# Kernel optimization log

Hardware: AMD Instinct MI355X
Metric: run time of the kernel (lower is better)

The kernel has to match this reference:

```python
import jax, jax.numpy as jnp
import numpy as np

D = 1024
H = 4096  # int(dim * mlp_ratio)
E = 8
B, N = 2, 2048


def setup_inputs() -> dict:
    key = jax.random.key(0)
    ks = jax.random.split(key, 5)
    x = jax.random.normal(ks[0], (B, N, D), dtype=jnp.float32)
    # torch Linear weights, stored pre-transposed for right-multiplication
    W1 = jax.random.normal(ks[1], (E, D, H), dtype=jnp.float32) / np.sqrt(D)
    W2 = jax.random.normal(ks[2], (E, H, D), dtype=jnp.float32) / np.sqrt(H)
    Wg = jax.random.normal(ks[3], (D, E), dtype=jnp.float32) / np.sqrt(D)
    bg = jax.random.normal(ks[4], (E,), dtype=jnp.float32) * 0.01
    return {"x": x, "W1": W1, "W2": W2, "Wg": Wg, "bg": bg}


def reference(x, W1, W2, Wg, bg):
    b, n, d = x.shape
    e = Wg.shape[1]
    xf = x.reshape(b * n, d)                      # [T, D]
    logits = xf @ Wg + bg                         # [T, E]
    one_hot = jax.nn.one_hot(jnp.argmax(logits, axis=-1), e, dtype=x.dtype)  # [T, E]
    # Dense all-experts compute (faithful to the original module)
    h = jax.nn.gelu(jnp.einsum('td,edh->eth', xf, W1), approximate=True)     # [E, T, H]
    y = jnp.einsum('eth,ehd->etd', h, W2)                                    # [E, T, D]
    out = jnp.einsum('etd,te->td', y, one_hot)                               # top-1 combine
    return out.reshape(b, n, d)
```

## Files before the change

kernel.cpp:

```cpp
#include <hip/hip_runtime.h>
#include <hip/hip_bf16.h>

#define Dq 1024
#define Hq 4096
#define Tq 4096
#define MAXTILES 40
#define NSTEP 16

#define XB_OFF 65536
#define HC_OFF (XB_OFF + Tq * Dq * 2)
#define WT_OFF (HC_OFF + MAXTILES * 128 * Hq * 2)

#define M_NT 0
#define M_CNT 8
#define M_POFF 16
#define M_CUR 32
#define M_TE 64
#define M_TR 128
#define M_EXP 512
#define M_PERM 4608

typedef __attribute__((ext_vector_type(8))) short bf16x8;
typedef __attribute__((ext_vector_type(4))) float f32x4;

__device__ __forceinline__ short f2bf(float f) {
    __hip_bfloat16 h = __float2bfloat16(f);
    return *reinterpret_cast<short*>(&h);
}

__device__ __forceinline__ float gelu_tanh(float x) {
    float u = 0.7978845608028654f * (x + 0.044715f * x * x * x);
    return x / (1.0f + __expf(-2.0f * u));
}

typedef __attribute__((address_space(1))) const void gvoid;
typedef __attribute__((address_space(3))) void lvoid;
__device__ __forceinline__ void glds16(const void* g, void* l) {
    __builtin_amdgcn_global_load_lds((gvoid*)g, (lvoid*)l, 16, 0, 0);
}

__global__ void k_init(int* meta) {
    int i = blockIdx.x * 256 + threadIdx.x;
    if (i < M_PERM + MAXTILES * 128) meta[i] = 0;
}

__global__ void k_tr(const float* __restrict__ in, short* __restrict__ out, int R, int C) {
    __shared__ float t[64][65];
    int e = blockIdx.z;
    int c0 = blockIdx.x * 64;
    int r0 = blockIdx.y * 64;
    const float* ine = in + (size_t)e * R * C;
    short* oute = out + (size_t)e * R * C;
    int tt = threadIdx.x;
    int lr = tt >> 4;
    int lc = (tt & 15) * 4;
#pragma unroll
    for (int p = 0; p < 4; ++p) {
        int r = p * 16 + lr;
        float4 v = *(const float4*)(ine + (size_t)(r0 + r) * C + c0 + lc);
        t[r][lc] = v.x; t[r][lc + 1] = v.y; t[r][lc + 2] = v.z; t[r][lc + 3] = v.w;
    }
    __syncthreads();
#pragma unroll
    for (int p = 0; p < 4; ++p) {
        int c = p * 16 + lr;
        short4 s;
        s.x = f2bf(t[lc][c]); s.y = f2bf(t[lc + 1][c]);
        s.z = f2bf(t[lc + 2][c]); s.w = f2bf(t[lc + 3][c]);
        *(short4*)(oute + (size_t)(c0 + c) * R + r0 + lc) = s;
    }
}

__global__ void k_route(const float* __restrict__ x, const float* __restrict__ Wg,
                        const float* __restrict__ bg, int* meta, short* __restrict__ xb) {
    int wave = threadIdx.x >> 6;
    int lane = threadIdx.x & 63;
    int t = blockIdx.x * 4 + wave;
    const float* xr = x + (size_t)t * Dq;
    float acc[8];
#pragma unroll
    for (int e = 0; e < 8; ++e) acc[e] = 0.0f;
#pragma unroll
    for (int j = 0; j < 16; ++j) {
        int d = j * 64 + lane;
        float xv = xr[d];
        xb[(size_t)t * Dq + d] = f2bf(xv);
        float4 w0 = *(const float4*)(Wg + (size_t)d * 8);
        float4 w1 = *(const float4*)(Wg + (size_t)d * 8 + 4);
        acc[0] += xv * w0.x; acc[1] += xv * w0.y; acc[2] += xv * w0.z; acc[3] += xv * w0.w;
        acc[4] += xv * w1.x; acc[5] += xv * w1.y; acc[6] += xv * w1.z; acc[7] += xv * w1.w;
    }
#pragma unroll
    for (int e = 0; e < 8; ++e) {
#pragma unroll
        for (int off = 32; off > 0; off >>= 1) acc[e] += __shfl_xor(acc[e], off);
    }
    if (lane == 0) {
        float best = acc[0] + bg[0];
        int be = 0;
#pragma unroll
        for (int e = 1; e < 8; ++e) {
            float v = acc[e] + bg[e];
            if (v > best) { best = v; be = e; }
        }
        meta[M_EXP + t] = be;
        atomicAdd(&meta[M_CNT + be], 1);
    }
}

__global__ void k_scan(int* meta) {
    if (threadIdx.x != 0) return;
    int off = 0, nt = 0;
    for (int e = 0; e < 8; ++e) {
        meta[M_POFF + e] = off;
        int c = meta[M_CNT + e];
        int m = (c + 127) / 128;
        for (int j = 0; j < m; ++j) {
            meta[M_TE + nt] = e;
            meta[M_TR + nt] = off + j * 128;
            ++nt;
        }
        off += m * 128;
    }
    meta[M_POFF + 8] = off;
    meta[M_NT] = nt;
}

__global__ void k_scatter(int* meta) {
    int t = blockIdx.x * 256 + threadIdx.x;
    if (t >= Tq) return;
    int e = meta[M_EXP + t];
    int pos = atomicAdd(&meta[M_CUR + e], 1);
    meta[M_PERM + meta[M_POFF + e] + pos] = t;
}

#define GEMM_SETUP()                                                           \
    int tt = threadIdx.x, w = tt >> 6, lane = tt & 63;                         \
    int fr = lane & 15, fg = lane >> 4;                                        \
    int rlo = lane >> 3;                                                       \
    int csw = ((lane & 7) ^ rlo) * 8;                                          \
    int ldsOff[4];                                                             \
    _Pragma("unroll")                                                          \
    for (int s = 0; s < 4; ++s) ldsOff[s] = (s * 32 + w * 8) * 64;             \
    int wm = (w >> 1) * 64, wn = (w & 1) * 64;                                 \
    int aoff[2][4], boff[2][4];                                                \
    _Pragma("unroll")                                                          \
    for (int s2 = 0; s2 < 2; ++s2)                                             \
      _Pragma("unroll")                                                        \
      for (int f = 0; f < 4; ++f) {                                            \
        int c = s2 * 4 + fg;                                                   \
        int m = wm + f * 16 + fr;                                              \
        aoff[s2][f] = m * 64 + ((c ^ (m & 7)) * 8);                            \
        int n = wn + f * 16 + fr;                                              \
        boff[s2][f] = n * 64 + ((c ^ (n & 7)) * 8);                            \
      }                                                                        \
    f32x4 acc[4][4];                                                           \
    _Pragma("unroll")                                                          \
    for (int a = 0; a < 4; ++a)                                                \
      _Pragma("unroll")                                                        \
      for (int b = 0; b < 4; ++b) acc[a][b] = (f32x4){0.f, 0.f, 0.f, 0.f};

#define KLOOP()                                                                \
  _Pragma("unroll")                                                            \
  for (int t = 0; t < NSTEP; ++t) {                                            \
    __syncthreads();                                                           \
    bf16x8 af[2][4], bv[2][4];                                                 \
    _Pragma("unroll")                                                          \
    for (int s2 = 0; s2 < 2; ++s2)                                             \
      _Pragma("unroll")                                                        \
      for (int f = 0; f < 4; ++f) {                                            \
        af[s2][f] = *(const bf16x8*)(&As[aoff[s2][f]]);                        \
        bv[s2][f] = *(const bf16x8*)(&Bs[boff[s2][f]]);                        \
      }                                                                        \
    __syncthreads();                                                           \
    if (t + 1 < NSTEP) {                                                       \
      _Pragma("unroll")                                                        \
      for (int s = 0; s < 4; ++s) {                                            \
        glds16(aSrc[s] + (t + 1) * 64, As + ldsOff[s]);                        \
        glds16(bSrc[s] + (t + 1) * 64, Bs + ldsOff[s]);                        \
      }                                                                        \
    }                                                                          \
    __builtin_amdgcn_sched_barrier(0);                                         \
    __builtin_amdgcn_s_setprio(1);                                             \
    _Pragma("unroll")                                                          \
    for (int s2 = 0; s2 < 2; ++s2)                                             \
      _Pragma("unroll")                                                        \
      for (int fm = 0; fm < 4; ++fm)                                           \
        _Pragma("unroll")                                                      \
        for (int fn = 0; fn < 4; ++fn)                                         \
          acc[fm][fn] = __builtin_amdgcn_mfma_f32_16x16x32_bf16(               \
              af[s2][fm], bv[s2][fn], acc[fm][fn], 0, 0, 0);                   \
    __builtin_amdgcn_s_setprio(0);                                             \
  }

__global__ __launch_bounds__(256, 3) void k_gemm1(const short* __restrict__ xb,
                                                  const short* __restrict__ W1T,
                                                  const int* __restrict__ meta,
                                                  short* __restrict__ Hc) {
    __shared__ short As[128 * 64];
    __shared__ short Bs[128 * 64];
    int hw = blockIdx.x;
    int xcd = hw & 7, q = hw >> 3;
    int mt = q >> 2;
    int n0 = (xcd * 4 + (q & 3)) * 128;
    if (mt >= meta[M_NT]) return;
    int e = meta[M_TE + mt];
    int i0 = meta[M_TR + mt];
    const int* perm = meta + M_PERM;

    GEMM_SETUP()

    const short* aSrc[4];
    const short* bSrc[4];
#pragma unroll
    for (int s = 0; s < 4; ++s) {
        int row = s * 32 + w * 8 + rlo;
        aSrc[s] = xb + (size_t)perm[i0 + row] * Dq + csw;
        bSrc[s] = W1T + ((size_t)e * Hq + n0 + row) * Dq + csw;
    }

#pragma unroll
    for (int s = 0; s < 4; ++s) {
        glds16(aSrc[s], As + ldsOff[s]);
        glds16(bSrc[s], Bs + ldsOff[s]);
    }

    KLOOP()

#pragma unroll
    for (int fm = 0; fm < 4; ++fm) {
        int rbase = i0 + wm + fm * 16 + fg * 4;
#pragma unroll
        for (int fn = 0; fn < 4; ++fn) {
            int col = n0 + wn + fn * 16 + fr;
#pragma unroll
            for (int p = 0; p < 4; ++p) {
                float v = gelu_tanh(acc[fm][fn][p]);
                Hc[(size_t)(rbase + p) * Hq + col] = f2bf(v);
            }
        }
    }
}

__global__ __launch_bounds__(256, 3) void k_gemm2(const short* __restrict__ Hc,
                                                  const short* __restrict__ W2T,
                                                  const int* __restrict__ meta,
                                                  float* __restrict__ out) {
    __shared__ short As[128 * 64];
    __shared__ short Bs[128 * 64];
    int hw = blockIdx.x;
    int xcd = hw & 7, q = hw >> 3;
    int mt = q >> 2;
    int sk = q & 3;
    int n0 = xcd * 128;
    int kbase = sk * (Hq / 4);
    if (mt >= meta[M_NT]) return;
    int e = meta[M_TE + mt];
    int i0 = meta[M_TR + mt];
    const int* perm = meta + M_PERM;
    int vend = meta[M_POFF + e] + meta[M_CNT + e];

    GEMM_SETUP()

    const short* aSrc[4];
    const short* bSrc[4];
#pragma unroll
    for (int s = 0; s < 4; ++s) {
        int row = s * 32 + w * 8 + rlo;
        aSrc[s] = Hc + (size_t)(i0 + row) * Hq + kbase + csw;
        bSrc[s] = W2T + ((size_t)e * Dq + n0 + row) * Hq + kbase + csw;
    }

#pragma unroll
    for (int s = 0; s < 4; ++s) {
        glds16(aSrc[s], As + ldsOff[s]);
        glds16(bSrc[s], Bs + ldsOff[s]);
    }

    KLOOP()

#pragma unroll
    for (int fm = 0; fm < 4; ++fm) {
        int rbase = i0 + wm + fm * 16 + fg * 4;
#pragma unroll
        for (int p = 0; p < 4; ++p) {
            int i = rbase + p;
            if (i < vend) {
                int tok = perm[i];
#pragma unroll
                for (int fn = 0; fn < 4; ++fn) {
                    int col = n0 + wn + fn * 16 + fr;
                    atomicAdd(&out[(size_t)tok * Dq + col], acc[fm][fn][p]);
                }
            }
        }
    }
}

extern "C" void kernel_launch(void* const* d_in, const int* in_sizes, int n_in,
                              void* d_out, int out_size, void* d_ws, size_t ws_size,
                              hipStream_t stream) {
    const float* x  = (const float*)d_in[0];
    const float* W1 = (const float*)d_in[1];
    const float* W2 = (const float*)d_in[2];
    const float* Wg = (const float*)d_in[3];
    const float* bg = (const float*)d_in[4];
    float* out = (float*)d_out;
    int* meta = (int*)d_ws;
    short* xb = (short*)((char*)d_ws + XB_OFF);
    short* Hc = (short*)((char*)d_ws + HC_OFF);
    short* WT = (short*)((char*)d_ws + WT_OFF);

    k_init<<<38, 256, 0, stream>>>(meta);
    hipMemsetAsync(d_out, 0, (size_t)Tq * Dq * 4, stream);
    k_route<<<Tq / 4, 256, 0, stream>>>(x, Wg, bg, meta, xb);
    k_scan<<<1, 64, 0, stream>>>(meta);
    k_scatter<<<Tq / 256, 256, 0, stream>>>(meta);
    k_tr<<<dim3(Hq / 64, Dq / 64, 8), 256, 0, stream>>>(W1, WT, Dq, Hq);
    k_gemm1<<<1280, 256, 0, stream>>>(xb, WT, meta, Hc);
    k_tr<<<dim3(Dq / 64, Hq / 64, 8), 256, 0, stream>>>(W2, WT, Hq, Dq);
    k_gemm2<<<1280, 256, 0, stream>>>(Hc, WT, meta, out);
}
```

Baseline: 294.4 us.

## Double-buffer LDS in grouped GEMMs and halve split-K in second GEMM

Both grouped GEMM kernels now use two LDS buffers, so the global-to-LDS loads for the next K step are issued before computing on the current one. The old scheme read fragments into registers and then synchronised before loading. Explicit vmcnt waits and raw barriers replace the paired __syncthreads. The K step is also split into two phases to cut register pressure. gemm1 remaps blocks so tiles sharing the same weight column group sit together, and gemm2 moves from 4-way to 2-way split-K with 640 blocks, reducing atomic traffic into the output. Occupancy drops from 3 to 2 blocks per CU because of the doubled LDS use.

Measured after the change: 310.0 us. 1.05x slower.

```diff
diff --git a/kernel.cpp b/kernel.cpp
--- a/kernel.cpp
+++ b/kernel.cpp
@@ -5,7 +5,6 @@
 #define Hq 4096
 #define Tq 4096
 #define MAXTILES 40
-#define NSTEP 16
 
 #define XB_OFF 65536
 #define HC_OFF (XB_OFF + Tq * Dq * 2)
@@ -38,6 +37,9 @@
 __device__ __forceinline__ void glds16(const void* g, void* l) {
     __builtin_amdgcn_global_load_lds((gvoid*)g, (lvoid*)l, 16, 0, 0);
 }
+
+#define WAITVM_(N) asm volatile("s_waitcnt vmcnt(" #N ")" ::: "memory")
+#define WAITVM(N) WAITVM_(N)
 
 __global__ void k_init(int* meta) {
     int i = blockIdx.x * 256 + threadIdx.x;
@@ -158,51 +160,60 @@
     _Pragma("unroll")                                                          \
     for (int a = 0; a < 4; ++a)                                                \
       _Pragma("unroll")                                                        \
-      for (int b = 0; b < 4; ++b) acc[a][b] = (f32x4){0.f, 0.f, 0.f, 0.f};
-
-#define KLOOP()                                                                \
-  _Pragma("unroll")                                                            \
-  for (int t = 0; t < NSTEP; ++t) {                                            \
-    __syncthreads();                                                           \
-    bf16x8 af[2][4], bv[2][4];                                                 \
-    _Pragma("unroll")                                                          \
-    for (int s2 = 0; s2 < 2; ++s2)                                             \
+      for (int b = 0; b < 2 * 2; ++b) acc[a][b] = (f32x4){0.f, 0.f, 0.f, 0.f};
+
+#define PHASE(S2, P)                                                           \
+  {                                                                            \
+    bf16x8 af[4], bv[4];                                                       \
+    _Pragma("unroll")                                                          \
+    for (int f = 0; f < 4; ++f) {                                              \
+      af[f] = *(const bf16x8*)(&As[(P) * 8192 + aoff[S2][f]]);                 \
+      bv[f] = *(const bf16x8*)(&Bs[(P) * 8192 + boff[S2][f]]);                 \
+    }                                                                          \
+    __builtin_amdgcn_s_barrier();                                              \
+    asm volatile("s_waitcnt lgkmcnt(0)" ::: "memory");                         \
+    __builtin_amdgcn_sched_barrier(0);                                         \
+    __builtin_amdgcn_s_setprio(1);                                             \
+    _Pragma("unroll")                                                          \
+    for (int fm = 0; fm < 4; ++fm)                                             \
       _Pragma("unroll")                                                        \
-      for (int f = 0; f < 4; ++f) {                                            \
-        af[s2][f] = *(const bf16x8*)(&As[aoff[s2][f]]);                        \
-        bv[s2][f] = *(const bf16x8*)(&Bs[boff[s2][f]]);                        \
-      }                                                                        \
-    __syncthreads();                                                           \
-    if (t + 1 < NSTEP) {                                                       \
+      for (int fn = 0; fn < 4; ++fn)                                           \
+        acc[fm][fn] = __builtin_amdgcn_mfma_f32_16x16x32_bf16(                 \
+            af[fm], bv[fn], acc[fm][fn], 0, 0, 0);                             \
+    __builtin_amdgcn_s_setprio(0);                                             \
+    __builtin_amdgcn_s_barrier();                                              \
+    asm volatile("" ::: "memory");                                             \
+  }
+
+#define KSTEP(T, NSTEP)                                                        \
+  {                                                                            \
+    const int P = (T) & 1;                                                     \
+    if ((T) + 1 < (NSTEP)) {                                                   \
       _Pragma("unroll")                                                        \
       for (int s = 0; s < 4; ++s) {                                            \
-        glds16(aSrc[s] + (t + 1) * 64, As + ldsOff[s]);                        \
-        glds16(bSrc[s] + (t + 1) * 64, Bs + ldsOff[s]);                        \
+        glds16(aSrc[s] + ((T) + 1) * 64, As + (1 - P) * 8192 + ldsOff[s]);     \
+        glds16(bSrc[s] + ((T) + 1) * 64, Bs + (1 - P) * 8192 + ldsOff[s]);     \
       }                                                                        \
+      WAITVM(8);                                                               \
+    } else {                                                                   \
+      WAITVM(0);                                                               \
     }                                                                          \
-    __builtin_amdgcn_sched_barrier(0);                                         \
-    __builtin_amdgcn_s_setprio(1);                                             \
-    _Pragma("unroll")                                                          \
-    for (int s2 = 0; s2 < 2; ++s2)                                             \
-      _Pragma("unroll")                                                        \
-      for (int fm = 0; fm < 4; ++fm)                                           \
-        _Pragma("unroll")                                                      \
-        for (int fn = 0; fn < 4; ++fn)                                         \
-          acc[fm][fn] = __builtin_amdgcn_mfma_f32_16x16x32_bf16(               \
-              af[s2][fm], bv[s2][fn], acc[fm][fn], 0, 0, 0);                   \
-    __builtin_amdgcn_s_setprio(0);                                             \
+    __builtin_amdgcn_s_barrier();                                              \
+    asm volatile("" ::: "memory");                                             \
+    PHASE(0, P)                                                                \
+    PHASE(1, P)                                                                \
   }
 
-__global__ __launch_bounds__(256, 3) void k_gemm1(const short* __restrict__ xb,
+__global__ __launch_bounds__(256, 2) void k_gemm1(const short* __restrict__ xb,
                                                   const short* __restrict__ W1T,
                                                   const int* __restrict__ meta,
                                                   short* __restrict__ Hc) {
-    __shared__ short As[128 * 64];
-    __shared__ short Bs[128 * 64];
+    __shared__ short As[2 * 8192];
+    __shared__ short Bs[2 * 8192];
     int hw = blockIdx.x;
     int xcd = hw & 7, q = hw >> 3;
-    int mt = q >> 2;
-    int n0 = (xcd * 4 + (q & 3)) * 128;
+    int mt = q % 40;
+    int n0 = (xcd * 4 + q / 40) * 128;
     if (mt >= meta[M_NT]) return;
     int e = meta[M_TE + mt];
     int i0 = meta[M_TR + mt];
@@ -225,7 +236,8 @@
         glds16(bSrc[s], Bs + ldsOff[s]);
     }
 
-    KLOOP()
+#pragma unroll 2
+    for (int t = 0; t < 16; ++t) KSTEP(t, 16)
 
 #pragma unroll
     for (int fm = 0; fm < 4; ++fm) {
@@ -242,18 +254,18 @@
     }
 }
 
-__global__ __launch_bounds__(256, 3) void k_gemm2(const short* __restrict__ Hc,
+__global__ __launch_bounds__(256, 2) void k_gemm2(const short* __restrict__ Hc,
                                                   const short* __restrict__ W2T,
                                                   const int* __restrict__ meta,
                                                   float* __restrict__ out) {
-    __shared__ short As[128 * 64];
-    __shared__ short Bs[128 * 64];
+    __shared__ short As[2 * 8192];
+    __shared__ short Bs[2 * 8192];
     int hw = blockIdx.x;
     int xcd = hw & 7, q = hw >> 3;
-    int mt = q >> 2;
-    int sk = q & 3;
+    int mt = q >> 1;
+    int sk = q & 1;
     int n0 = xcd * 128;
-    int kbase = sk * (Hq / 4);
+    int kbase = sk * (Hq / 2);
     if (mt >= meta[M_NT]) return;
     int e = meta[M_TE + mt];
     int i0 = meta[M_TR + mt];
@@ -277,7 +289,8 @@
         glds16(bSrc[s], Bs + ldsOff[s]);
     }
 
-    KLOOP()
+#pragma unroll 2
+    for (int t = 0; t < 32; ++t) KSTEP(t, 32)
 
 #pragma unroll
     for (int fm = 0; fm < 4; ++fm) {
@@ -319,5 +332,5 @@
     k_tr<<<dim3(Hq / 64, Dq / 64, 8), 256, 0, stream>>>(W1, WT, Dq, Hq);
     k_gemm1<<<1280, 256, 0, stream>>>(xb, WT, meta, Hc);
     k_tr<<<dim3(Dq / 64, Hq / 64, 8), 256, 0, stream>>>(W2, WT, Hq, Dq);
-    k_gemm2<<<1280, 256, 0, stream>>>(Hc, WT, meta, out);
-}
+    k_gemm2<<<640, 256, 0, stream>>>(Hc, WT, meta, out);
+}
```
